# Kernel tuning notes

Hardware: AMD Instinct MI355X
Metric: run time of the kernel (lower is better)

The kernel has to match this reference:

```python
import jax, jax.numpy as jnp
import numpy as np

HEAD_NUM = 16
MASK_FILL = 100000.0  # source uses +1e5 on masked entries (not -inf)


def setup_inputs() -> dict:
    key = jax.random.key(0)
    k1, k2, k3, k4, k5 = jax.random.split(key, 5)
    B, S, E = 2, 2048, 1024
    scale = 0.02
    return {
        "x": jax.random.normal(k1, (B, S, E), dtype=jnp.float32),
        "W_atten": jax.random.normal(k2, (E, 3 * E), dtype=jnp.float32) * scale,
        "b_atten": jax.random.normal(k3, (3 * E,), dtype=jnp.float32) * scale,
        "W_proj": jax.random.normal(k4, (E, E), dtype=jnp.float32) * scale,
        "b_proj": jax.random.normal(k5, (E,), dtype=jnp.float32) * scale,
    }


def reference(x, W_atten, b_atten, W_proj, b_proj):
    B, S, E = x.shape
    H = HEAD_NUM
    hd = E // H
    # QKV projection: [B, S, 3E]
    qkv = x @ W_atten + b_atten
    # reshape [B, S, H, 3*hd] -> [B, H, S, 3*hd], chunk into q,k,v [B,H,S,hd]
    qkv = jnp.transpose(qkv.reshape(B, S, H, 3 * hd), (0, 2, 1, 3))
    q, k, v = jnp.split(qkv, 3, axis=-1)
    # raw scores, NO 1/sqrt(dk) scaling (faithful to source)
    w = jnp.einsum("bhqd,bhkd->bhqk", q, k)
    # causal mask applied as w*mask + (1-mask)*1e5 (faithful to source)
    mask = jnp.tril(jnp.ones((S, S), dtype=w.dtype))
    w = w * mask + (1.0 - mask) * MASK_FILL
    # softmax over dim=1 == HEAD axis (faithful to source quirk)
    w = jax.nn.softmax(w, axis=1)
    # attn_drop: identity in eval mode
    a = jnp.einsum("bhqk,bhkd->bhqd", w, v)  # [B,H,S,hd]
    a = jnp.transpose(a, (0, 2, 1, 3)).reshape(B, S, E)
    h = a @ W_proj + b_proj
    # resi_drop: identity in eval mode
    return h
```

## Files before the change

### kernel.cpp

```cpp
#include <hip/hip_runtime.h>

#define DI __device__ __forceinline__

typedef __attribute__((ext_vector_type(8))) short s16x8;
typedef __attribute__((ext_vector_type(4))) short s16x4;
typedef __attribute__((ext_vector_type(4))) float f32x4;

DI unsigned short f2bf(float f){
  unsigned u = __float_as_uint(f);
  u = (u + 0x7FFFu + ((u >> 16) & 1u)) >> 16;
  return (unsigned short)u;
}
DI float bf2f(unsigned short h){
  return __uint_as_float(((unsigned)h) << 16);
}
DI float exp2i(float x){ float r; asm("v_exp_f32 %0, %1" : "=v"(r) : "v"(x)); return r; }

DI void gll16(const void* g, void* l){
  __builtin_amdgcn_global_load_lds((const __attribute__((address_space(1))) void*)g,
                                   (__attribute__((address_space(3))) void*)l, 16, 0, 0);
}

#define VMCNT(n) asm volatile("s_waitcnt vmcnt(" #n ")" ::: "memory")
#define SB() __builtin_amdgcn_sched_barrier(0)

__global__ void prep_kernel(const float* __restrict__ x, unsigned short* __restrict__ xb,
                            const float* __restrict__ Wa, unsigned short* __restrict__ WaT,
                            const float* __restrict__ Wp, unsigned short* __restrict__ WpT)
{
  __shared__ float t[32][33];
  int blk = blockIdx.x, tid = threadIdx.x;
  if (blk < 2048){
    int i = blk * 256 + tid;
    const float4* p = (const float4*)x + (size_t)i * 2;
    float4 a = p[0], b = p[1];
    s16x8 o;
    o[0] = (short)f2bf(a.x); o[1] = (short)f2bf(a.y); o[2] = (short)f2bf(a.z); o[3] = (short)f2bf(a.w);
    o[4] = (short)f2bf(b.x); o[5] = (short)f2bf(b.y); o[6] = (short)f2bf(b.z); o[7] = (short)f2bf(b.w);
    ((s16x8*)xb)[i] = o;
  } else {
    const float* in; unsigned short* out; int R, C, bx, by;
    if (blk < 5120){
      int k = blk - 2048; in = Wa; out = WaT; R = 1024; C = 3072; bx = k % 96; by = k / 96;
    } else {
      int k = blk - 5120; in = Wp; out = WpT; R = 1024; C = 1024; bx = k % 32; by = k / 32;
    }
    int c0 = bx * 32, r0 = by * 32;
    int tx = tid & 31, ty = tid >> 5;
    #pragma unroll
    for (int i = 0; i < 4; i++)
      t[ty + i*8][tx] = in[(size_t)(r0 + ty + i*8) * C + c0 + tx];
    __syncthreads();
    #pragma unroll
    for (int i = 0; i < 4; i++)
      out[(size_t)(c0 + ty + i*8) * R + r0 + tx] = f2bf(t[tx][ty + i*8]);
  }
}

template<int MODE, int BM>
__launch_bounds__(256)
__global__ void gemm_kernel(const unsigned short* __restrict__ A,
                            const unsigned short* __restrict__ Wt,
                            const float* __restrict__ bias,
                            int N,
                            unsigned short* __restrict__ qb,
                            unsigned short* __restrict__ kb,
                            unsigned short* __restrict__ vt,
                            float* __restrict__ out)
{
  constexpr int MI = BM / 32;
  constexpr int AC = BM / 32;
  const int K = 1024;
  __shared__ __align__(16) unsigned short Sm[BM*64 + 128*64];
  unsigned short* As = Sm;
  unsigned short* Bs = Sm + BM*64;

  int lin = blockIdx.y * gridDim.x + blockIdx.x;
  int chunk = (gridDim.x * gridDim.y) >> 3;
  int v = (lin & 7) * chunk + (lin >> 3);
  int bx = v % gridDim.x, by = v / gridDim.x;
  int m0 = by * BM, n0 = bx * 128;

  int tid = threadIdx.x;
  int lane = tid & 63, w = tid >> 6;
  int row_l = lane & 15, kgrp = lane >> 4;
  int wm = (w >> 1) * (MI * 16), wn = (w & 1) * 64;

  const unsigned short* asrc[AC];
  const unsigned short* bsrc[4];
  int ldsoA[AC], ldsoB[4];
  int chnk = (lane & 7) ^ (lane >> 3);
  #pragma unroll
  for (int c4 = 0; c4 < AC; c4++){
    int r = c4*32 + w*8 + (lane >> 3);
    asrc[c4] = A + (size_t)(m0 + r) * K + chnk*8;
    ldsoA[c4] = (c4*32 + w*8) * 64;
  }
  #pragma unroll
  for (int c4 = 0; c4 < 4; c4++){
    int r = c4*32 + w*8 + (lane >> 3);
    bsrc[c4] = Wt + (size_t)(n0 + r) * K + chnk*8;
    ldsoB[c4] = (c4*32 + w*8) * 64;
  }
  int eA[MI], eB[4];
  #pragma unroll
  for (int i = 0; i < MI; i++){
    int ra = wm + i*16 + row_l;
    eA[i] = (ra*64 + kgrp*8) ^ ((ra & 7) << 3);
  }
  #pragma unroll
  for (int i = 0; i < 4; i++){
    int rb = wn + i*16 + row_l;
    eB[i] = (rb*64 + kgrp*8) ^ ((rb & 7) << 3);
  }

  f32x4 acc[MI][4];
  #pragma unroll
  for (int i = 0; i < MI; i++)
    #pragma unroll
    for (int j = 0; j < 4; j++)
      acc[i][j] = (f32x4){0.f, 0.f, 0.f, 0.f};

  for (int k0 = 0; k0 < K; k0 += 64){
    #pragma unroll
    for (int c4 = 0; c4 < AC; c4++)
      gll16(asrc[c4] + k0, (void*)(As + ldsoA[c4]));
    #pragma unroll
    for (int c4 = 0; c4 < 4; c4++)
      gll16(bsrc[c4] + k0, (void*)(Bs + ldsoB[c4]));
    __syncthreads();
    #pragma unroll
    for (int kc = 0; kc < 2; kc++){
      s16x8 af[MI], bfr[4];
      #pragma unroll
      for (int mi = 0; mi < MI; mi++)
        af[mi] = *(const s16x8*)&As[eA[mi] ^ (kc*32)];
      #pragma unroll
      for (int ni = 0; ni < 4; ni++)
        bfr[ni] = *(const s16x8*)&Bs[eB[ni] ^ (kc*32)];
      #pragma unroll
      for (int mi = 0; mi < MI; mi++)
        #pragma unroll
        for (int ni = 0; ni < 4; ni++)
          acc[mi][ni] = __builtin_amdgcn_mfma_f32_16x16x32_bf16(af[mi], bfr[ni], acc[mi][ni], 0, 0, 0);
    }
    __syncthreads();
  }

  if (MODE == 0){
    unsigned long long* ldsT = (unsigned long long*)Sm;
    #pragma unroll
    for (int mi = 0; mi < MI; mi++){
      #pragma unroll
      for (int ni = 0; ni < 4; ni++){
        int np = wn + ni*16 + row_l;
        int gc = n0 + np;
        int hh = gc / 192, cc = gc % 192;
        float bia = bias[gc];
        if (cc < 128){
          #pragma unroll
          for (int j = 0; j < 4; j++){
            int gr = m0 + wm + mi*16 + kgrp*4 + j;
            float v2 = acc[mi][ni][j] + bia;
            if (cc < 64){
              qb[(size_t)gr * 1024 + hh*64 + cc] = f2bf(v2 * 1.44269504f);
            } else {
              int d = cc - 64; int b = gr >> 11, s = gr & 2047;
              int kt = s >> 6, kk = s & 63;
              kb[(size_t)((b*16 + hh)*32 + kt) * 4096 + ((kk*64 + d) ^ ((kk & 7) << 3))] = f2bf(v2);
            }
          }
        } else {
          float v0 = acc[mi][ni][0] + bia, v1 = acc[mi][ni][1] + bia;
          float v2 = acc[mi][ni][2] + bia, v3 = acc[mi][ni][3] + bia;
          unsigned lo, hi;
          asm("v_cvt_pk_bf16_f32 %0, %1, %2" : "=v"(lo) : "v"(v0), "v"(v1));
          asm("v_cvt_pk_bf16_f32 %0, %1, %2" : "=v"(hi) : "v"(v2), "v"(v3));
          int mq = (wm + mi*16 + kgrp*4) >> 2;
          ldsT[np*32 + (mq ^ ((np & 7) << 2))] = ((unsigned long long)hi << 32) | (unsigned long long)lo;
        }
      }
    }
    __syncthreads();
    int bb = m0 >> 11, s_base = m0 & 2047;
    for (int item = tid; item < 2048; item += 256){
      int np = item >> 4;
      int gcv = n0 + np;
      int cc = gcv % 192;
      if (cc < 128) continue;
      int d = cc - 128, hh = gcv / 192;
      int sub = (item >> 3) & 1;
      int c = item & 7;
      int mq0 = sub*16 + c*2;
      s16x8 val = *(const s16x8*)&Sm[np*128 + ((mq0 ^ ((np & 7) << 2)) << 2)];
      size_t base = ((size_t)((bb*16 + hh)*32) + (s_base >> 6) + sub) * 4096 + d*64 + ((c ^ (d & 7)) << 3);
      *(s16x8*)&vt[base] = val;
    }
  } else {
    #pragma unroll
    for (int mi = 0; mi < MI; mi++){
      #pragma unroll
      for (int ni = 0; ni < 4; ni++){
        #pragma unroll
        for (int j = 0; j < 4; j++){
          int gr = m0 + wm + mi*16 + kgrp*4 + j;
          int gc = n0 + wn + ni*16 + row_l;
          out[(size_t)gr * N + gc] = acc[mi][ni][j] + bias[gc];
        }
      }
    }
  }
}

__global__ void sufv_kernel(const unsigned short* __restrict__ vt, float* __restrict__ sufv){
  __shared__ float tot[4][64];
  int bh = blockIdx.x;
  int tid = threadIdx.x;
  int tq = tid >> 6, d = tid & 63;
  const unsigned short* base = vt + (size_t)bh * 32 * 4096;
  float s[8];
  float run = 0.f;
  for (int j = 7; j >= 0; j--){
    int t = tq*8 + j;
    float rs = 0.f;
    #pragma unroll
    for (int c = 0; c < 8; c++){
      int idx = (d*64 + c*8) ^ ((d & 7) << 3);
      s16x8 v = *(const s16x8*)&base[(size_t)t*4096 + idx];
      #pragma unroll
      for (int e = 0; e < 8; e++) rs += bf2f((unsigned short)v[e]);
    }
    run += rs; s[j] = run;
  }
  tot[tq][d] = run;
  __syncthreads();
  float carry = 0.f;
  for (int t2 = tq+1; t2 < 4; t2++) carry += tot[t2][d];
  #pragma unroll
  for (int j = 0; j < 8; j++)
    sufv[((size_t)bh*33 + tq*8 + j)*64 + d] = s[j] + carry;
  if (tid < 64) sufv[((size_t)bh*33 + 32)*64 + tid] = 0.f;
}

__launch_bounds__(256)
__global__ void dpass_kernel(const unsigned short* __restrict__ qbuf,
                             const unsigned short* __restrict__ kb,
                             unsigned short* __restrict__ invb)
{
  __shared__ unsigned short Kst[4][4096];
  int bid = blockIdx.x;
  int blk = (bid & 7) * 132 + (bid >> 3);
  int b = blk / 528, t = blk % 528;
  int kt = (int)(32.5f - sqrtf(1056.25f - 2.f*t));
  while (kt*(65-kt)/2 > t) kt--;
  while ((kt+1)*(64-kt)/2 <= t) kt++;
  int qt = kt + (t - kt*(65-kt)/2);

  int tid = threadIdx.x, lane = tid & 63, w = tid >> 6;
  int row_l = lane & 15, kgrp = lane >> 4;

  const unsigned short* ktb = kb + ((size_t)(b*16)*32 + kt) * 4096;
  int sgoff = (w*128 + lane)*8;

  auto stage = [&](int hh, int buf){
    const unsigned short* src = ktb + (size_t)hh * 131072;
    gll16(src + sgoff,       (void*)(&Kst[buf][0] + w*1024));
    gll16(src + sgoff + 512, (void*)(&Kst[buf][0] + w*1024 + 512));
  };

  int e0[4];
  #pragma unroll
  for (int ks = 0; ks < 4; ks++){
    int row = ks*16 + row_l;
    e0[ks] = (row*64 + kgrp*8) ^ ((row & 7) << 3);
  }

  stage(0, 0);
  stage(1, 1);

  f32x4 esum[4];
  #pragma unroll
  for (int ks = 0; ks < 4; ks++) esum[ks] = (f32x4){0.f,0.f,0.f,0.f};

  const unsigned short* qrow_p = qbuf + (size_t)(b*2048 + qt*64 + w*16 + row_l) * 1024;
  s16x8 qf0 = *(const s16x8*)&qrow_p[kgrp*8];
  s16x8 qf1 = *(const s16x8*)&qrow_p[32 + kgrp*8];

  for (int h = 0; h < 16; h++){
    s16x8 qn0, qn1;
    if (h < 15){
      qn0 = *(const s16x8*)&qrow_p[(h+1)*64 + kgrp*8];
      qn1 = *(const s16x8*)&qrow_p[(h+1)*64 + 32 + kgrp*8];
    }
    if (h + 2 < 16) stage(h+2, (h+2) & 3);
    SB();
    if (h < 14)      VMCNT(8);
    else if (h < 15) VMCNT(6);
    else             VMCNT(2);
    SB();
    __builtin_amdgcn_s_barrier();
    SB();

    const unsigned short* kl = &Kst[h & 3][0];
    #pragma unroll
    for (int ks = 0; ks < 4; ks++){
      s16x8 a0 = *(const s16x8*)&kl[e0[ks]];
      s16x8 a1 = *(const s16x8*)&kl[e0[ks] ^ 32];
      f32x4 sc = __builtin_amdgcn_mfma_f32_16x16x32_bf16(a0, qf0, (f32x4){0.f,0.f,0.f,0.f}, 0, 0, 0);
      sc = __builtin_amdgcn_mfma_f32_16x16x32_bf16(a1, qf1, sc, 0, 0, 0);
      #pragma unroll
      for (int j = 0; j < 4; j++) esum[ks][j] += exp2i(sc[j]);
    }
    if (h < 15){ qf0 = qn0; qf1 = qn1; }
  }

  int qcol = qt*64 + w*16 + row_l;
  unsigned short* dst = invb + (size_t)b*4194304 + (size_t)qcol*2048 + kt*64 + kgrp*4;
  #pragma unroll
  for (int ks = 0; ks < 4; ks++){
    float r0 = 1.f/esum[ks][0], r1 = 1.f/esum[ks][1];
    float r2 = 1.f/esum[ks][2], r3 = 1.f/esum[ks][3];
    unsigned lo, hi;
    asm("v_cvt_pk_bf16_f32 %0, %1, %2" : "=v"(lo) : "v"(r0), "v"(r1));
    asm("v_cvt_pk_bf16_f32 %0, %1, %2" : "=v"(hi) : "v"(r2), "v"(r3));
    uint2 pk; pk.x = lo; pk.y = hi;
    *(uint2*)&dst[ks*16] = pk;
  }
}

__launch_bounds__(256)
__global__ void pv_kernel(const unsigned short* __restrict__ qbuf,
                          const unsigned short* __restrict__ kb,
                          const unsigned short* __restrict__ vt,
                          const unsigned short* __restrict__ invb,
                          const float* __restrict__ sufv,
                          unsigned short* __restrict__ ab)
{
  __shared__ unsigned short Kst[3][4096];
  __shared__ unsigned short Vst[2][4096];
  __shared__ unsigned short Wsh[4][1152];

  int bid = blockIdx.x;
  int blk = ((bid & 7) << 6) | (bid >> 3);
  int i = blk & 15;
  int h = (blk >> 4) & 15;
  int b = blk >> 8;

  int tid = threadIdx.x, lane = tid & 63, w = tid >> 6;
  int row_l = lane & 15, kgrp = lane >> 4;

  const unsigned short* KT = kb + (size_t)((b*16 + h)*32) * 4096;
  const unsigned short* VT = vt + (size_t)((b*16 + h)*32) * 4096;
  int sgoff = (w*128 + lane)*8;
  unsigned short* Wsw = &Wsh[w][0];

  int eK[4];
  #pragma unroll
  for (int ks = 0; ks < 4; ks++){
    int row = ks*16 + row_l;
    eK[ks] = (row*64 + kgrp*8) ^ ((row & 7) << 3);
  }

  auto stageK = [&](int kt, int buf){
    gll16(KT + (size_t)kt*4096 + sgoff,       (void*)(&Kst[buf][0] + w*1024));
    gll16(KT + (size_t)kt*4096 + sgoff + 512, (void*)(&Kst[buf][0] + w*1024 + 512));
  };
  auto stageV = [&](int kt, int buf){
    gll16(VT + (size_t)kt*4096 + sgoff,       (void*)(&Vst[buf][0] + w*1024));
    gll16(VT + (size_t)kt*4096 + sgoff + 512, (void*)(&Vst[buf][0] + w*1024 + 512));
  };

  auto run = [&](int qt, int k1t){
    int q0 = qt * 64;
    int qv = q0 + w*16 + row_l;
    const unsigned short* qrow_p = qbuf + (size_t)(b*2048 + qv) * 1024 + h*64;
    s16x8 qf0 = *(const s16x8*)&qrow_p[kgrp*8];
    s16x8 qf1 = *(const s16x8*)&qrow_p[32 + kgrp*8];
    SB();
    const unsigned short* ivrow = invb + (size_t)b*4194304 + (size_t)qv*2048 + kgrp*4;

    f32x4 pvv[4];
    #pragma unroll
    for (int d = 0; d < 4; d++) pvv[d] = (f32x4){0.f,0.f,0.f,0.f};

    __syncthreads();
    stageK(0, 0);
    stageV(0, 0);
    s16x4 i1[4];
    #pragma unroll
    for (int ks = 0; ks < 4; ks++) i1[ks] = *(const s16x4*)&ivrow[ks*16];
    if (1 < k1t) stageK(1, 1);
    SB();

    for (int kt = 0; kt < k1t; kt++){
      bool nx1 = (kt + 1 < k1t), nx2 = (kt + 2 < k1t);
      bool first = (kt == 0);

      s16x4 icur[4];
      #pragma unroll
      for (int ks = 0; ks < 4; ks++) icur[ks] = i1[ks];
      if (nx1){
        #pragma unroll
        for (int ks = 0; ks < 4; ks++) i1[ks] = *(const s16x4*)&ivrow[(kt+1)*64 + ks*16];
      }
      SB();
      if (first){
        if (nx1) VMCNT(10);
        else     VMCNT(4);
      } else {
        if (nx1) VMCNT(4);
        else     VMCNT(0);
      }
      SB();
      __builtin_amdgcn_s_barrier();
      SB();
      if (nx2) stageK(kt+2, (kt+2) % 3);
      if (nx1) stageV(kt+1, (kt+1) & 1);
      SB();

      const unsigned short* kl = &Kst[kt % 3][0];
      const unsigned short* vl = &Vst[kt & 1][0];
      f32x4 sc[4];
      #pragma unroll
      for (int ks = 0; ks < 4; ks++){
        s16x8 a0 = *(const s16x8*)&kl[eK[ks]];
        s16x8 a1 = *(const s16x8*)&kl[eK[ks] ^ 32];
        sc[ks] = __builtin_amdgcn_mfma_f32_16x16x32_bf16(a0, qf0, (f32x4){0.f,0.f,0.f,0.f}, 0, 0, 0);
        sc[ks] = __builtin_amdgcn_mfma_f32_16x16x32_bf16(a1, qf1, sc[ks], 0, 0, 0);
      }

      if (kt == qt){
        int kbase = kt*64 + kgrp*4;
        #pragma unroll
        for (int ks = 0; ks < 4; ks++){
          #pragma unroll
          for (int j = 0; j < 4; j++){
            float wv = exp2i(sc[ks][j]) * bf2f((unsigned short)icur[ks][j]);
            sc[ks][j] = (kbase + ks*16 + j > qv) ? 0.0625f : wv;
          }
          unsigned lo, hi;
          asm("v_cvt_pk_bf16_f32 %0, %1, %2" : "=v"(lo) : "v"(sc[ks][0]), "v"(sc[ks][1]));
          asm("v_cvt_pk_bf16_f32 %0, %1, %2" : "=v"(hi) : "v"(sc[ks][2]), "v"(sc[ks][3]));
          uint2 pk2; pk2.x = lo; pk2.y = hi;
          *(uint2*)&Wsw[row_l*72 + ks*16 + kgrp*4] = pk2;
        }
      } else {
        #pragma unroll
        for (int ks = 0; ks < 4; ks++){
          #pragma unroll
          for (int j = 0; j < 4; j++)
            sc[ks][j] = exp2i(sc[ks][j]) * bf2f((unsigned short)icur[ks][j]);
          unsigned lo, hi;
          asm("v_cvt_pk_bf16_f32 %0, %1, %2" : "=v"(lo) : "v"(sc[ks][0]), "v"(sc[ks][1]));
          asm("v_cvt_pk_bf16_f32 %0, %1, %2" : "=v"(hi) : "v"(sc[ks][2]), "v"(sc[ks][3]));
          uint2 pk2; pk2.x = lo; pk2.y = hi;
          *(uint2*)&Wsw[row_l*72 + ks*16 + kgrp*4] = pk2;
        }
      }

      #pragma unroll
      for (int kc = 0; kc < 2; kc++){
        s16x8 af = *(const s16x8*)&Wsw[row_l*72 + kc*32 + kgrp*8];
        #pragma unroll
        for (int dq = 0; dq < 4; dq++){
          s16x8 vf = *(const s16x8*)&vl[eK[dq] ^ (kc*32)];
          pvv[dq] = __builtin_amdgcn_mfma_f32_16x16x32_bf16(af, vf, pvv[dq], 0, 0, 0);
        }
      }
    }

    int tsuf = qt + 1;
    #pragma unroll
    for (int dq = 0; dq < 4; dq++){
      int d = dq*16 + row_l;
      float suf = sufv[((size_t)(b*16 + h)*33 + tsuf)*64 + d];
      #pragma unroll
      for (int j = 0; j < 4; j++){
        int qo = q0 + w*16 + kgrp*4 + j;
        ab[(size_t)(b*2048 + qo)*1024 + h*64 + d] = f2bf(pvv[dq][j] + 0.0625f * suf);
      }
    }
  };

  run(i, i + 1);
  run(31 - i, 32 - i);
}

extern "C" void kernel_launch(void* const* d_in, const int* in_sizes, int n_in,
                              void* d_out, int out_size, void* d_ws, size_t ws_size,
                              hipStream_t stream) {
  (void)in_sizes; (void)n_in; (void)out_size; (void)ws_size;
  const float* x  = (const float*)d_in[0];
  const float* Wa = (const float*)d_in[1];
  const float* ba = (const float*)d_in[2];
  const float* Wp = (const float*)d_in[3];
  const float* bp = (const float*)d_in[4];
  float* out = (float*)d_out;

  char* ws = (char*)d_ws;
  size_t off = 0;
  auto alloc = [&](size_t bytes) -> void* {
    void* p = ws + off;
    off += (bytes + 255) & ~(size_t)255;
    return p;
  };
  unsigned short* xb   = (unsigned short*)alloc((size_t)4096*1024*2);
  unsigned short* WaT  = (unsigned short*)alloc((size_t)3072*1024*2);
  unsigned short* WpT  = (unsigned short*)alloc((size_t)1024*1024*2);
  unsigned short* qbuf = (unsigned short*)alloc((size_t)4096*1024*2);
  unsigned short* ktile= (unsigned short*)alloc((size_t)4096*1024*2);
  unsigned short* vtile= (unsigned short*)alloc((size_t)4096*1024*2);
  unsigned short* abuf = (unsigned short*)alloc((size_t)4096*1024*2);
  unsigned short* invb = (unsigned short*)alloc((size_t)2*2048*2048*2);
  float* sufv          = (float*)alloc((size_t)32*33*64*4);

  prep_kernel<<<6144, 256, 0, stream>>>(x, xb, Wa, WaT, Wp, WpT);

  gemm_kernel<0,128><<<dim3(24, 32), 256, 0, stream>>>(xb, WaT, ba, 3072, qbuf, ktile, vtile, nullptr);

  sufv_kernel<<<32, 256, 0, stream>>>(vtile, sufv);

  dpass_kernel<<<1056, 256, 0, stream>>>(qbuf, ktile, invb);

  pv_kernel<<<512, 256, 0, stream>>>(qbuf, ktile, vtile, invb, sufv, abuf);

  gemm_kernel<1,64><<<dim3(1024/128, 4096/64), 256, 0, stream>>>(abuf, WpT, bp, 1024, nullptr, nullptr, nullptr, out);
}
```

Before: 154.4 us.

## Process two tiles per barrier in dpass and pv pipelines

Both the denominator pass and the PV kernel now handle two heads or key tiles per loop iteration. Each iteration issues one barrier and stages two tiles ahead into 4-slot LDS ring buffers. The goal is to halve barrier and wait overhead and to give the scheduler more independent MFMA and exp work to overlap with the loads. In exchange, pv uses more LDS (K and V each grow to 4 slots), which may lower occupancy. Odd tile counts are handled by clamping redundant loads to the last tile.

```diff
diff --git a/kernel.cpp b/kernel.cpp
--- a/kernel.cpp
+++ b/kernel.cpp
@@ -250,11 +250,11 @@
   __shared__ unsigned short Kst[4][4096];
   int bid = blockIdx.x;
   int blk = (bid & 7) * 132 + (bid >> 3);
-  int b = blk / 528, t = blk % 528;
-  int kt = (int)(32.5f - sqrtf(1056.25f - 2.f*t));
-  while (kt*(65-kt)/2 > t) kt--;
-  while ((kt+1)*(64-kt)/2 <= t) kt++;
-  int qt = kt + (t - kt*(65-kt)/2);
+  int b = blk / 528, t0 = blk % 528;
+  int kt = (int)(32.5f - sqrtf(1056.25f - 2.f*t0));
+  while (kt*(65-kt)/2 > t0) kt--;
+  while ((kt+1)*(64-kt)/2 <= t0) kt++;
+  int qt = kt + (t0 - kt*(65-kt)/2);
 
   int tid = threadIdx.x, lane = tid & 63, w = tid >> 6;
   int row_l = lane & 15, kgrp = lane >> 4;
@@ -262,10 +262,10 @@
   const unsigned short* ktb = kb + ((size_t)(b*16)*32 + kt) * 4096;
   int sgoff = (w*128 + lane)*8;
 
-  auto stage = [&](int hh, int buf){
+  auto stage = [&](int hh){
     const unsigned short* src = ktb + (size_t)hh * 131072;
-    gll16(src + sgoff,       (void*)(&Kst[buf][0] + w*1024));
-    gll16(src + sgoff + 512, (void*)(&Kst[buf][0] + w*1024 + 512));
+    gll16(src + sgoff,       (void*)(&Kst[hh & 3][0] + w*1024));
+    gll16(src + sgoff + 512, (void*)(&Kst[hh & 3][0] + w*1024 + 512));
   };
 
   int e0[4];
@@ -275,43 +275,54 @@
     e0[ks] = (row*64 + kgrp*8) ^ ((row & 7) << 3);
   }
 
-  stage(0, 0);
-  stage(1, 1);
+  const unsigned short* qrow_p = qbuf + (size_t)(b*2048 + qt*64 + w*16 + row_l) * 1024;
+
+  stage(0); stage(1);
+  s16x8 qa0 = *(const s16x8*)&qrow_p[kgrp*8];
+  s16x8 qa1 = *(const s16x8*)&qrow_p[32 + kgrp*8];
+  s16x8 qb0 = *(const s16x8*)&qrow_p[64 + kgrp*8];
+  s16x8 qb1 = *(const s16x8*)&qrow_p[64 + 32 + kgrp*8];
+  SB();
 
   f32x4 esum[4];
   #pragma unroll
   for (int ks = 0; ks < 4; ks++) esum[ks] = (f32x4){0.f,0.f,0.f,0.f};
 
-  const unsigned short* qrow_p = qbuf + (size_t)(b*2048 + qt*64 + w*16 + row_l) * 1024;
-  s16x8 qf0 = *(const s16x8*)&qrow_p[kgrp*8];
-  s16x8 qf1 = *(const s16x8*)&qrow_p[32 + kgrp*8];
-
-  for (int h = 0; h < 16; h++){
-    s16x8 qn0, qn1;
-    if (h < 15){
-      qn0 = *(const s16x8*)&qrow_p[(h+1)*64 + kgrp*8];
-      qn1 = *(const s16x8*)&qrow_p[(h+1)*64 + 32 + kgrp*8];
-    }
-    if (h + 2 < 16) stage(h+2, (h+2) & 3);
+  for (int t = 0; t < 8; t++){
+    int h = 2*t;
+    s16x8 qn0, qn1, qn2, qn3;
+    if (t < 7){
+      qn0 = *(const s16x8*)&qrow_p[(h+2)*64 + kgrp*8];
+      qn1 = *(const s16x8*)&qrow_p[(h+2)*64 + 32 + kgrp*8];
+      qn2 = *(const s16x8*)&qrow_p[(h+3)*64 + kgrp*8];
+      qn3 = *(const s16x8*)&qrow_p[(h+3)*64 + 32 + kgrp*8];
+    }
     SB();
-    if (h < 14)      VMCNT(8);
-    else if (h < 15) VMCNT(6);
-    else             VMCNT(2);
+    if (t == 0)     VMCNT(8);
+    else if (t < 7) VMCNT(4);
+    else            VMCNT(0);
     SB();
     __builtin_amdgcn_s_barrier();
     SB();
-
-    const unsigned short* kl = &Kst[h & 3][0];
+    if (t < 7){ stage(h+2); stage(h+3); }
+    SB();
+
+    const unsigned short* kl0 = &Kst[h & 3][0];
+    const unsigned short* kl1 = &Kst[(h+1) & 3][0];
     #pragma unroll
     for (int ks = 0; ks < 4; ks++){
-      s16x8 a0 = *(const s16x8*)&kl[e0[ks]];
-      s16x8 a1 = *(const s16x8*)&kl[e0[ks] ^ 32];
-      f32x4 sc = __builtin_amdgcn_mfma_f32_16x16x32_bf16(a0, qf0, (f32x4){0.f,0.f,0.f,0.f}, 0, 0, 0);
-      sc = __builtin_amdgcn_mfma_f32_16x16x32_bf16(a1, qf1, sc, 0, 0, 0);
-      #pragma unroll
-      for (int j = 0; j < 4; j++) esum[ks][j] += exp2i(sc[j]);
-    }
-    if (h < 15){ qf0 = qn0; qf1 = qn1; }
+      s16x8 a0 = *(const s16x8*)&kl0[e0[ks]];
+      s16x8 a1 = *(const s16x8*)&kl0[e0[ks] ^ 32];
+      f32x4 sc = __builtin_amdgcn_mfma_f32_16x16x32_bf16(a0, qa0, (f32x4){0.f,0.f,0.f,0.f}, 0, 0, 0);
+      sc = __builtin_amdgcn_mfma_f32_16x16x32_bf16(a1, qa1, sc, 0, 0, 0);
+      s16x8 b0 = *(const s16x8*)&kl1[e0[ks]];
+      s16x8 b1 = *(const s16x8*)&kl1[e0[ks] ^ 32];
+      f32x4 sd = __builtin_amdgcn_mfma_f32_16x16x32_bf16(b0, qb0, (f32x4){0.f,0.f,0.f,0.f}, 0, 0, 0);
+      sd = __builtin_amdgcn_mfma_f32_16x16x32_bf16(b1, qb1, sd, 0, 0, 0);
+      #pragma unroll
+      for (int j = 0; j < 4; j++) esum[ks][j] += exp2i(sc[j]) + exp2i(sd[j]);
+    }
+    if (t < 7){ qa0 = qn0; qa1 = qn1; qb0 = qn2; qb1 = qn3; }
   }
 
   int qcol = qt*64 + w*16 + row_l;
@@ -336,8 +347,8 @@
                           const float* __restrict__ sufv,
                           unsigned short* __restrict__ ab)
 {
-  __shared__ unsigned short Kst[3][4096];
-  __shared__ unsigned short Vst[2][4096];
+  __shared__ unsigned short Kst[4][4096];
+  __shared__ unsigned short Vst[4][4096];
   __shared__ unsigned short Wsh[4][1152];
 
   int bid = blockIdx.x;
@@ -361,13 +372,13 @@
     eK[ks] = (row*64 + kgrp*8) ^ ((row & 7) << 3);
   }
 
-  auto stageK = [&](int kt, int buf){
-    gll16(KT + (size_t)kt*4096 + sgoff,       (void*)(&Kst[buf][0] + w*1024));
-    gll16(KT + (size_t)kt*4096 + sgoff + 512, (void*)(&Kst[buf][0] + w*1024 + 512));
+  auto stageK = [&](int kt, int slot){
+    gll16(KT + (size_t)kt*4096 + sgoff,       (void*)(&Kst[slot][0] + w*1024));
+    gll16(KT + (size_t)kt*4096 + sgoff + 512, (void*)(&Kst[slot][0] + w*1024 + 512));
   };
-  auto stageV = [&](int kt, int buf){
-    gll16(VT + (size_t)kt*4096 + sgoff,       (void*)(&Vst[buf][0] + w*1024));
-    gll16(VT + (size_t)kt*4096 + sgoff + 512, (void*)(&Vst[buf][0] + w*1024 + 512));
+  auto stageV = [&](int kt, int slot){
+    gll16(VT + (size_t)kt*4096 + sgoff,       (void*)(&Vst[slot][0] + w*1024));
+    gll16(VT + (size_t)kt*4096 + sgoff + 512, (void*)(&Vst[slot][0] + w*1024 + 512));
   };
 
   auto run = [&](int qt, int k1t){
@@ -383,43 +394,9 @@
     #pragma unroll
     for (int d = 0; d < 4; d++) pvv[d] = (f32x4){0.f,0.f,0.f,0.f};
 
-    __syncthreads();
-    stageK(0, 0);
-    stageV(0, 0);
-    s16x4 i1[4];
-    #pragma unroll
-    for (int ks = 0; ks < 4; ks++) i1[ks] = *(const s16x4*)&ivrow[ks*16];
-    if (1 < k1t) stageK(1, 1);
-    SB();
-
-    for (int kt = 0; kt < k1t; kt++){
-      bool nx1 = (kt + 1 < k1t), nx2 = (kt + 2 < k1t);
-      bool first = (kt == 0);
-
-      s16x4 icur[4];
-      #pragma unroll
-      for (int ks = 0; ks < 4; ks++) icur[ks] = i1[ks];
-      if (nx1){
-        #pragma unroll
-        for (int ks = 0; ks < 4; ks++) i1[ks] = *(const s16x4*)&ivrow[(kt+1)*64 + ks*16];
-      }
-      SB();
-      if (first){
-        if (nx1) VMCNT(10);
-        else     VMCNT(4);
-      } else {
-        if (nx1) VMCNT(4);
-        else     VMCNT(0);
-      }
-      SB();
-      __builtin_amdgcn_s_barrier();
-      SB();
-      if (nx2) stageK(kt+2, (kt+2) % 3);
-      if (nx1) stageV(kt+1, (kt+1) & 1);
-      SB();
-
-      const unsigned short* kl = &Kst[kt % 3][0];
-      const unsigned short* vl = &Vst[kt & 1][0];
+    auto compute_tile = [&](int kt, int slot, s16x4* icur){
+      const unsigned short* kl = &Kst[slot][0];
+      const unsigned short* vl = &Vst[slot][0];
       f32x4 sc[4];
       #pragma unroll
       for (int ks = 0; ks < 4; ks++){
@@ -428,7 +405,6 @@
         sc[ks] = __builtin_amdgcn_mfma_f32_16x16x32_bf16(a0, qf0, (f32x4){0.f,0.f,0.f,0.f}, 0, 0, 0);
         sc[ks] = __builtin_amdgcn_mfma_f32_16x16x32_bf16(a1, qf1, sc[ks], 0, 0, 0);
       }
-
       if (kt == qt){
         int kbase = kt*64 + kgrp*4;
         #pragma unroll
@@ -457,7 +433,6 @@
           *(uint2*)&Wsw[row_l*72 + ks*16 + kgrp*4] = pk2;
         }
       }
-
       #pragma unroll
       for (int kc = 0; kc < 2; kc++){
         s16x8 af = *(const s16x8*)&Wsw[row_l*72 + kc*32 + kgrp*8];
@@ -466,6 +441,61 @@
           s16x8 vf = *(const s16x8*)&vl[eK[dq] ^ (kc*32)];
           pvv[dq] = __builtin_amdgcn_mfma_f32_16x16x32_bf16(af, vf, pvv[dq], 0, 0, 0);
         }
+      }
+    };
+
+    int NT = (k1t + 1) >> 1;
+    int t1p = (1 < k1t) ? 1 : 0;
+
+    __syncthreads();
+    stageK(0, 0); stageK(t1p, 1);
+    stageV(0, 0); stageV(t1p, 1);
+    s16x4 iA[4], iB[4];
+    #pragma unroll
+    for (int ks = 0; ks < 4; ks++){
+      iA[ks] = *(const s16x4*)&ivrow[ks*16];
+      iB[ks] = *(const s16x4*)&ivrow[t1p*64 + ks*16];
+    }
+    SB();
+
+    for (int j = 0; j < NT; j++){
+      int t0 = 2*j;
+      bool t1v = (t0 + 1 < k1t);
+      bool nx = (j + 1 < NT);
+      int s0 = (t0+2 < k1t) ? t0+2 : k1t-1;
+      int s1 = (t0+3 < k1t) ? t0+3 : k1t-1;
+
+      s16x4 nA[4], nB[4];
+      if (nx){
+        #pragma unroll
+        for (int ks = 0; ks < 4; ks++){
+          nA[ks] = *(const s16x4*)&ivrow[s0*64 + ks*16];
+          nB[ks] = *(const s16x4*)&ivrow[s1*64 + ks*16];
+        }
+      }
+      SB();
+      if (j == 0){
+        if (nx) VMCNT(16);
+        else    VMCNT(8);
+      } else {
+        if (nx) VMCNT(8);
+        else    VMCNT(0);
+      }
+      SB();
+      __builtin_amdgcn_s_barrier();
+      SB();
+      if (nx){
+        stageK(s0, (t0+2) & 3); stageK(s1, (t0+3) & 3);
+        stageV(s0, (t0+2) & 3); stageV(s1, (t0+3) & 3);
+      }
+      SB();
+
+      compute_tile(t0, t0 & 3, iA);
+      if (t1v) compute_tile(t0 + 1, (t0 + 1) & 3, iB);
+
+      if (nx){
+        #pragma unroll
+        for (int ks = 0; ks < 4; ks++){ iA[ks] = nA[ks]; iB[ks] = nB[ks]; }
       }
     }
 
```

Result: slower. 162.0 us (+4.9%).

## Process two heads per barrier in dpass and raise MFMA priority in pv

Applied to the files above, without the earlier changes.

The denominator pass now handles two heads per loop iteration. This halves the number of barriers and waitcnt points and issues two independent MFMA chains to hide latency, and K staging for the next two heads now starts after the barrier. The PV kernel wraps its MFMA sections in s_setprio(1) so waves issuing matrix work get scheduling priority over waves doing exp and conversion. The cost is more registers for the extra Q fragments, and the reordered waitcnt values must still match the loads in flight.

```diff
diff --git a/kernel.cpp b/kernel.cpp
--- a/kernel.cpp
+++ b/kernel.cpp
@@ -250,11 +250,11 @@
   __shared__ unsigned short Kst[4][4096];
   int bid = blockIdx.x;
   int blk = (bid & 7) * 132 + (bid >> 3);
-  int b = blk / 528, t = blk % 528;
-  int kt = (int)(32.5f - sqrtf(1056.25f - 2.f*t));
-  while (kt*(65-kt)/2 > t) kt--;
-  while ((kt+1)*(64-kt)/2 <= t) kt++;
-  int qt = kt + (t - kt*(65-kt)/2);
+  int b = blk / 528, t0 = blk % 528;
+  int kt = (int)(32.5f - sqrtf(1056.25f - 2.f*t0));
+  while (kt*(65-kt)/2 > t0) kt--;
+  while ((kt+1)*(64-kt)/2 <= t0) kt++;
+  int qt = kt + (t0 - kt*(65-kt)/2);
 
   int tid = threadIdx.x, lane = tid & 63, w = tid >> 6;
   int row_l = lane & 15, kgrp = lane >> 4;
@@ -262,10 +262,10 @@
   const unsigned short* ktb = kb + ((size_t)(b*16)*32 + kt) * 4096;
   int sgoff = (w*128 + lane)*8;
 
-  auto stage = [&](int hh, int buf){
+  auto stage = [&](int hh){
     const unsigned short* src = ktb + (size_t)hh * 131072;
-    gll16(src + sgoff,       (void*)(&Kst[buf][0] + w*1024));
-    gll16(src + sgoff + 512, (void*)(&Kst[buf][0] + w*1024 + 512));
+    gll16(src + sgoff,       (void*)(&Kst[hh & 3][0] + w*1024));
+    gll16(src + sgoff + 512, (void*)(&Kst[hh & 3][0] + w*1024 + 512));
   };
 
   int e0[4];
@@ -275,43 +275,54 @@
     e0[ks] = (row*64 + kgrp*8) ^ ((row & 7) << 3);
   }
 
-  stage(0, 0);
-  stage(1, 1);
+  const unsigned short* qrow_p = qbuf + (size_t)(b*2048 + qt*64 + w*16 + row_l) * 1024;
+
+  stage(0); stage(1);
+  s16x8 qa0 = *(const s16x8*)&qrow_p[kgrp*8];
+  s16x8 qa1 = *(const s16x8*)&qrow_p[32 + kgrp*8];
+  s16x8 qb0 = *(const s16x8*)&qrow_p[64 + kgrp*8];
+  s16x8 qb1 = *(const s16x8*)&qrow_p[64 + 32 + kgrp*8];
+  SB();
 
   f32x4 esum[4];
   #pragma unroll
   for (int ks = 0; ks < 4; ks++) esum[ks] = (f32x4){0.f,0.f,0.f,0.f};
 
-  const unsigned short* qrow_p = qbuf + (size_t)(b*2048 + qt*64 + w*16 + row_l) * 1024;
-  s16x8 qf0 = *(const s16x8*)&qrow_p[kgrp*8];
-  s16x8 qf1 = *(const s16x8*)&qrow_p[32 + kgrp*8];
-
-  for (int h = 0; h < 16; h++){
-    s16x8 qn0, qn1;
-    if (h < 15){
-      qn0 = *(const s16x8*)&qrow_p[(h+1)*64 + kgrp*8];
-      qn1 = *(const s16x8*)&qrow_p[(h+1)*64 + 32 + kgrp*8];
-    }
-    if (h + 2 < 16) stage(h+2, (h+2) & 3);
+  for (int t = 0; t < 8; t++){
+    int h = 2*t;
+    s16x8 qn0, qn1, qn2, qn3;
+    if (t < 7){
+      qn0 = *(const s16x8*)&qrow_p[(h+2)*64 + kgrp*8];
+      qn1 = *(const s16x8*)&qrow_p[(h+2)*64 + 32 + kgrp*8];
+      qn2 = *(const s16x8*)&qrow_p[(h+3)*64 + kgrp*8];
+      qn3 = *(const s16x8*)&qrow_p[(h+3)*64 + 32 + kgrp*8];
+    }
     SB();
-    if (h < 14)      VMCNT(8);
-    else if (h < 15) VMCNT(6);
-    else             VMCNT(2);
+    if (t == 0)     VMCNT(8);
+    else if (t < 7) VMCNT(4);
+    else            VMCNT(0);
     SB();
     __builtin_amdgcn_s_barrier();
     SB();
-
-    const unsigned short* kl = &Kst[h & 3][0];
+    if (t < 7){ stage(h+2); stage(h+3); }
+    SB();
+
+    const unsigned short* kl0 = &Kst[h & 3][0];
+    const unsigned short* kl1 = &Kst[(h+1) & 3][0];
     #pragma unroll
     for (int ks = 0; ks < 4; ks++){
-      s16x8 a0 = *(const s16x8*)&kl[e0[ks]];
-      s16x8 a1 = *(const s16x8*)&kl[e0[ks] ^ 32];
-      f32x4 sc = __builtin_amdgcn_mfma_f32_16x16x32_bf16(a0, qf0, (f32x4){0.f,0.f,0.f,0.f}, 0, 0, 0);
-      sc = __builtin_amdgcn_mfma_f32_16x16x32_bf16(a1, qf1, sc, 0, 0, 0);
-      #pragma unroll
-      for (int j = 0; j < 4; j++) esum[ks][j] += exp2i(sc[j]);
-    }
-    if (h < 15){ qf0 = qn0; qf1 = qn1; }
+      s16x8 a0 = *(const s16x8*)&kl0[e0[ks]];
+      s16x8 a1 = *(const s16x8*)&kl0[e0[ks] ^ 32];
+      f32x4 sc = __builtin_amdgcn_mfma_f32_16x16x32_bf16(a0, qa0, (f32x4){0.f,0.f,0.f,0.f}, 0, 0, 0);
+      sc = __builtin_amdgcn_mfma_f32_16x16x32_bf16(a1, qa1, sc, 0, 0, 0);
+      s16x8 b0 = *(const s16x8*)&kl1[e0[ks]];
+      s16x8 b1 = *(const s16x8*)&kl1[e0[ks] ^ 32];
+      f32x4 sd = __builtin_amdgcn_mfma_f32_16x16x32_bf16(b0, qb0, (f32x4){0.f,0.f,0.f,0.f}, 0, 0, 0);
+      sd = __builtin_amdgcn_mfma_f32_16x16x32_bf16(b1, qb1, sd, 0, 0, 0);
+      #pragma unroll
+      for (int j = 0; j < 4; j++) esum[ks][j] += exp2i(sc[j]) + exp2i(sd[j]);
+    }
+    if (t < 7){ qa0 = qn0; qa1 = qn1; qb0 = qn2; qb1 = qn3; }
   }
 
   int qcol = qt*64 + w*16 + row_l;
@@ -421,6 +432,7 @@
       const unsigned short* kl = &Kst[kt % 3][0];
       const unsigned short* vl = &Vst[kt & 1][0];
       f32x4 sc[4];
+      __builtin_amdgcn_s_setprio(1);
       #pragma unroll
       for (int ks = 0; ks < 4; ks++){
         s16x8 a0 = *(const s16x8*)&kl[eK[ks]];
@@ -428,6 +440,7 @@
         sc[ks] = __builtin_amdgcn_mfma_f32_16x16x32_bf16(a0, qf0, (f32x4){0.f,0.f,0.f,0.f}, 0, 0, 0);
         sc[ks] = __builtin_amdgcn_mfma_f32_16x16x32_bf16(a1, qf1, sc[ks], 0, 0, 0);
       }
+      __builtin_amdgcn_s_setprio(0);
 
       if (kt == qt){
         int kbase = kt*64 + kgrp*4;
@@ -458,6 +471,7 @@
         }
       }
 
+      __builtin_amdgcn_s_setprio(1);
       #pragma unroll
       for (int kc = 0; kc < 2; kc++){
         s16x8 af = *(const s16x8*)&Wsw[row_l*72 + kc*32 + kgrp*8];
@@ -467,6 +481,7 @@
           pvv[dq] = __builtin_amdgcn_mfma_f32_16x16x32_bf16(af, vf, pvv[dq], 0, 0, 0);
         }
       }
+      __builtin_amdgcn_s_setprio(0);
     }
 
     int tsuf = qt + 1;
```

After: 153.6 us. About the same (-0.5%).
